# Optimization experiments

Hardware: AMD Instinct MI355X
Metric: run time of the kernel (lower is better)

Reference implementation:

```python
import jax, jax.numpy as jnp
import numpy as np

K = 5  # k_neighbors


def _pairwise_sq(a, b):
    # (B,N,3),(B,M,3) -> (B,N,M) squared euclidean distances (matmul form)
    d = (jnp.sum(a * a, -1)[:, :, None] + jnp.sum(b * b, -1)[:, None, :]
         - 2.0 * jnp.einsum('bnd,bmd->bnm', a, b))
    return jnp.maximum(d, 0.0)


def _knn_indices(points, k):
    # (B,N,3) -> (B,N,k) indices of k nearest neighbors, excluding self
    d = _pairwise_sq(points, points)
    _, idx = jax.lax.top_k(-d, k + 1)
    return idx[:, :, 1:]


def _gather_neighbors(feats, idx):
    # feats (B,N,C), idx (B,N,k) -> (B,N,k,C)
    B, N, k = idx.shape
    flat = jnp.take_along_axis(feats, idx.reshape(B, N * k, 1), axis=1)
    return flat.reshape(B, N, k, feats.shape[-1])


def setup_inputs() -> dict:
    key = jax.random.key(0)
    ks = jax.random.split(key, 8)
    B, N, M = 8, 4096, 4000
    return {
        'Y': jax.random.normal(ks[0], (B, N, 3), jnp.float32),
        'X': jax.random.normal(ks[1], (B, M, 3), jnp.float32),
        'R_pred': jax.random.normal(ks[2], (B, 3, 3), jnp.float32),
        't_pred': jax.random.normal(ks[3], (B, 3), jnp.float32),
        'R_gt': jax.random.normal(ks[4], (B, 3, 3), jnp.float32),
        't_gt': jax.random.normal(ks[5], (B, 3), jnp.float32),
        'X_hat': jax.random.normal(ks[6], (B, N, 3), jnp.float32),
        'delta': jax.random.normal(ks[7], (B, N, 3), jnp.float32),
    }


def reference(Y, X, R_pred, t_pred, R_gt, t_gt, X_hat, delta):
    lam_rot, lam_trans, lam_rmse = 1.0, 1.0, 1.0
    lam_align, lam_disp, lam_deform, lam_lap = 1.0, 0.01, 0.1, 0.1

    # --- rigid losses ---
    # rotation geodesic: R_delta = R_pred^T @ R_gt
    R_delta = jnp.einsum('bij,bik->bjk', R_pred, R_gt)
    tr = jnp.trace(R_delta, axis1=1, axis2=2)
    cos_a = jnp.clip((tr - 1.0) / 2.0, -1.0 + 1e-7, 1.0 - 1e-7)
    L_rot = jnp.mean(jnp.arccos(cos_a))

    L_trans = jnp.mean(jnp.linalg.norm(t_pred - t_gt, axis=1))

    # Y @ R^T + t
    Y_pred = jnp.einsum('bnd,bkd->bnk', Y, R_pred) + t_pred[:, None, :]
    Y_gt = jnp.einsum('bnd,bkd->bnk', Y, R_gt) + t_gt[:, None, :]
    L_rmse = jnp.mean(jnp.sqrt(jnp.mean(jnp.sum((Y_pred - Y_gt) ** 2, -1), axis=1)))

    rigid = lam_rot * L_rot + lam_trans * L_trans + lam_rmse * L_rmse

    # --- non-rigid losses ---
    Y_rigid = Y_pred  # apply_rigid_transform(Y, R_pred, t_pred)

    # alignment: N != M -> kNN matching of X_hat against X
    d_align = _pairwise_sq(X_hat, X)          # (B,N,M)
    knn_d = -jax.lax.top_k(-d_align, K)[0]    # (B,N,K) smallest distances
    L_align = jnp.mean(knn_d)

    L_disp = jnp.mean(jnp.sum(delta ** 2, -1))

    # kNN graph on Y_rigid (original builds it twice with identical result)
    idx = _knn_indices(Y_rigid, K)            # (B,N,K)

    Yn = _gather_neighbors(Y_rigid, idx)      # (B,N,K,3)
    Xn = _gather_neighbors(X_hat, idx)
    edge_diff = (Xn - X_hat[:, :, None, :]) - (Yn - Y_rigid[:, :, None, :])
    L_deform = jnp.mean(jnp.sum(edge_diff ** 2, -1))

    dn = _gather_neighbors(delta, idx)        # (B,N,K,3)
    lap = delta - jnp.mean(dn, axis=2)
    L_lap = jnp.mean(jnp.sum(lap ** 2, -1))

    non_rigid = (lam_align * L_align + lam_disp * L_disp
                 + lam_deform * L_deform + lam_lap * L_lap)
    total = rigid + non_rigid

    return jnp.stack([total, rigid, non_rigid, L_rot, L_trans, L_rmse,
                      L_align, L_disp, L_deform, L_lap])
```

## Files before the change

### kernel.cpp

```cpp
#include <hip/hip_runtime.h>
#include <math.h>

#define BB 8
#define NN 4096
#define MM 4000
#define KK 5
#define NWAVE 8
#define QG 128
#define CH 512
#define NPAD 4096
#define SCAN_BLOCKS ((NN / QG) * BB * 2)

#define ACC_ROT    0
#define ACC_TRANS  1
#define ACC_ALIGN  2
#define ACC_DISP   3
#define ACC_DEFORM 4
#define ACC_LAP    5
#define ACC_RMSE   6
#define ACC_COUNT  14

#define INFF __int_as_float(0x7F800000)

__device__ __forceinline__ float waveReduceSum(float v) {
#pragma unroll
    for (int off = 32; off > 0; off >>= 1) v += __shfl_down(v, off, 64);
    return v;
}

template<bool SELF, bool PACK>
__device__ __forceinline__ void proc1(float4 c, int midx, int q,
                                      float ca, float cbq, float cc,
                                      float& b0, float& b1, float& b2,
                                      float& b3, float& b4) {
    float sc = fmaf(c.x, ca, fmaf(c.y, cbq, fmaf(c.z, cc, c.w)));
    float v;
    if (PACK) {
        unsigned pk = (__float_as_uint(sc) & 0xFFFFF000u) | (unsigned)midx;
        v = __uint_as_float(pk);
        if (SELF) v = (midx == q) ? INFF : v;
    } else {
        v = sc;
    }
    float n0 = fminf(b0, v);
    float n1 = __builtin_amdgcn_fmed3f(v, b0, b1);
    float n2 = __builtin_amdgcn_fmed3f(v, b1, b2);
    float n3 = __builtin_amdgcn_fmed3f(v, b2, b3);
    float n4 = __builtin_amdgcn_fmed3f(v, b3, b4);
    b0 = n0; b1 = n1; b2 = n2; b3 = n3; b4 = n4;
}

template<bool SELF, bool PACK>
__device__ __forceinline__ void scanGlob2(const float4* __restrict__ cb, int tc,
                                          float a0, float b0c, float c0, int q0,
                                          float a1, float b1c, float c1, int q1,
                                          float& x0, float& x1, float& x2,
                                          float& x3, float& x4,
                                          float& y0, float& y1, float& y2,
                                          float& y3, float& y4) {
    float4 A[8], B[8];
#pragma unroll
    for (int j = 0; j < 8; ++j) A[j] = cb[tc + j];

    for (int t0 = 0; t0 < CH; t0 += 16) {
#pragma unroll
        for (int j = 0; j < 8; ++j) B[j] = cb[tc + t0 + 8 + j];
#pragma unroll
        for (int j = 0; j < 8; ++j) {
            proc1<SELF, PACK>(A[j], tc + t0 + j, q0, a0, b0c, c0, x0, x1, x2, x3, x4);
            proc1<SELF, PACK>(A[j], tc + t0 + j, q1, a1, b1c, c1, y0, y1, y2, y3, y4);
        }
        if (t0 + 16 < CH) {
#pragma unroll
            for (int j = 0; j < 8; ++j) A[j] = cb[tc + t0 + 16 + j];
        }
#pragma unroll
        for (int j = 0; j < 8; ++j) {
            proc1<SELF, PACK>(B[j], tc + t0 + 8 + j, q0, a0, b0c, c0, x0, x1, x2, x3, x4);
            proc1<SELF, PACK>(B[j], tc + t0 + 8 + j, q1, a1, b1c, c1, y0, y1, y2, y3, y4);
        }
    }
}

__global__ void k_prep(const float* __restrict__ Y, const float* __restrict__ X,
                       const float* __restrict__ Rp, const float* __restrict__ tp,
                       const float* __restrict__ Rg, const float* __restrict__ tg,
                       const float* __restrict__ dl,
                       float4* __restrict__ YrP, float4* __restrict__ XP,
                       float* __restrict__ acc) {
    int b = blockIdx.x >> 4;
    int n = ((blockIdx.x & 15) << 8) + threadIdx.x;
    size_t base = ((size_t)b * NN + n) * 3;
    float yx = Y[base + 0], yy = Y[base + 1], yz = Y[base + 2];

    float rp[9], rg[9], tpv[3], tgv[3];
#pragma unroll
    for (int i = 0; i < 9; ++i) { rp[i] = Rp[b * 9 + i]; rg[i] = Rg[b * 9 + i]; }
#pragma unroll
    for (int i = 0; i < 3; ++i) { tpv[i] = tp[b * 3 + i]; tgv[i] = tg[b * 3 + i]; }

    float p[3], dr2 = 0.f;
#pragma unroll
    for (int k = 0; k < 3; ++k) {
        float pv = fmaf(yx, rp[k * 3 + 0], fmaf(yy, rp[k * 3 + 1], fmaf(yz, rp[k * 3 + 2], tpv[k])));
        float gv = fmaf(yx, rg[k * 3 + 0], fmaf(yy, rg[k * 3 + 1], fmaf(yz, rg[k * 3 + 2], tgv[k])));
        p[k] = pv;
        float dd = pv - gv;
        dr2 = fmaf(dd, dd, dr2);
    }
    YrP[(size_t)b * NPAD + n] =
        make_float4(p[0], p[1], p[2], fmaf(p[0], p[0], fmaf(p[1], p[1], p[2] * p[2])));

    float4 xe;
    if (n < MM) {
        size_t xb = ((size_t)b * MM + n) * 3;
        float x0 = X[xb + 0], x1 = X[xb + 1], x2 = X[xb + 2];
        xe = make_float4(x0, x1, x2, fmaf(x0, x0, fmaf(x1, x1, x2 * x2)));
    } else {
        xe = make_float4(0.f, 0.f, 0.f, INFF);
    }
    XP[(size_t)b * NPAD + n] = xe;

    float d0 = dl[base + 0], d1 = dl[base + 1], d2 = dl[base + 2];
    float dsq = d0 * d0 + d1 * d1 + d2 * d2;

    dr2 = waveReduceSum(dr2);
    dsq = waveReduceSum(dsq);
    if ((threadIdx.x & 63) == 0) {
        atomicAdd(&acc[ACC_RMSE + b], dr2);
        atomicAdd(&acc[ACC_DISP], dsq);
    }

    if (threadIdx.x == 0 && (blockIdx.x & 15) == 0) {
        float tr = 0.f;
#pragma unroll
        for (int i = 0; i < 9; ++i) tr += rp[i] * rg[i];
        float c = (tr - 1.f) * 0.5f;
        c = fminf(fmaxf(c, -1.f + 1e-7f), 1.f - 1e-7f);
        float dx = tpv[0] - tgv[0], dy = tpv[1] - tgv[1], dz = tpv[2] - tgv[2];
        atomicAdd(&acc[ACC_ROT], acosf(c));
        atomicAdd(&acc[ACC_TRANS], sqrtf(dx * dx + dy * dy + dz * dz));
    }
}

__device__ void finalize(const float* acc, float* out) {
    float a[ACC_COUNT];
#pragma unroll
    for (int i = 0; i < ACC_COUNT; ++i)
        a[i] = __hip_atomic_load(&acc[i], __ATOMIC_RELAXED, __HIP_MEMORY_SCOPE_AGENT);
    float L_rot = a[ACC_ROT] / BB;
    float L_trans = a[ACC_TRANS] / BB;
    float L_rmse = 0.f;
#pragma unroll
    for (int b = 0; b < BB; ++b) L_rmse += sqrtf(a[ACC_RMSE + b] / NN);
    L_rmse /= BB;
    float L_align = a[ACC_ALIGN] / ((float)BB * NN * KK);
    float L_disp = a[ACC_DISP] / ((float)BB * NN);
    float L_def = a[ACC_DEFORM] / ((float)BB * NN * KK);
    float L_lap = a[ACC_LAP] / ((float)BB * NN);
    float rigid = L_rot + L_trans + L_rmse;
    float nr = L_align + 0.01f * L_disp + 0.1f * L_def + 0.1f * L_lap;
    out[0] = rigid + nr; out[1] = rigid; out[2] = nr;
    out[3] = L_rot; out[4] = L_trans; out[5] = L_rmse;
    out[6] = L_align; out[7] = L_disp; out[8] = L_def; out[9] = L_lap;
}

#define MERGE_STEP(W) { float d = md[W][l][pp##W]; if (d < best) { best = d; bw = W; } }
#define MERGE_ADV()  { pp0 += (bw == 0); pp1 += (bw == 1); pp2 += (bw == 2); pp3 += (bw == 3); \
                       pp4 += (bw == 4); pp5 += (bw == 5); pp6 += (bw == 6); pp7 += (bw == 7); }

__global__ __launch_bounds__(512, 4) void k_scan(const float* __restrict__ Xh,
                                                 const float4* __restrict__ XP,
                                                 const float4* __restrict__ YrP,
                                                 const float* __restrict__ dl,
                                                 float* __restrict__ acc,
                                                 unsigned* __restrict__ doneCnt,
                                                 float* __restrict__ out) {
    __shared__ float md[NWAVE][QG][6];
    int tid = threadIdx.x, wave = tid >> 6, lane = tid & 63;
    int qg = blockIdx.x, b = blockIdx.y, mode = blockIdx.z;
    int q0 = qg * QG + lane, q1 = q0 + 64;

    const float4* cbG = (mode == 0 ? XP : YrP) + (size_t)b * NPAD;

    float qx0, qy0, qz0, qx1, qy1, qz1;
    if (mode == 0) {
        size_t a0 = ((size_t)b * NN + q0) * 3;
        size_t a1 = ((size_t)b * NN + q1) * 3;
        qx0 = Xh[a0 + 0]; qy0 = Xh[a0 + 1]; qz0 = Xh[a0 + 2];
        qx1 = Xh[a1 + 0]; qy1 = Xh[a1 + 1]; qz1 = Xh[a1 + 2];
    } else {
        float4 p0 = cbG[q0], p1 = cbG[q1];
        qx0 = p0.x; qy0 = p0.y; qz0 = p0.z;
        qx1 = p1.x; qy1 = p1.y; qz1 = p1.z;
    }

    float x0 = INFF, x1 = INFF, x2 = INFF, x3 = INFF, x4 = INFF;
    float y0 = INFF, y1 = INFF, y2 = INFF, y3 = INFF, y4 = INFF;
    int tc = wave * CH;
    if (mode == 0) {
        scanGlob2<false, false>(cbG, tc,
                                -2.f * qx0, -2.f * qy0, -2.f * qz0, 0,
                                -2.f * qx1, -2.f * qy1, -2.f * qz1, 0,
                                x0, x1, x2, x3, x4, y0, y1, y2, y3, y4);
    } else if (wave == (qg >> 2)) {
        scanGlob2<true, true>(cbG, tc,
                              -2.f * qx0, -2.f * qy0, -2.f * qz0, q0,
                              -2.f * qx1, -2.f * qy1, -2.f * qz1, q1,
                              x0, x1, x2, x3, x4, y0, y1, y2, y3, y4);
    } else {
        scanGlob2<false, true>(cbG, tc,
                               -2.f * qx0, -2.f * qy0, -2.f * qz0, q0,
                               -2.f * qx1, -2.f * qy1, -2.f * qz1, q1,
                               x0, x1, x2, x3, x4, y0, y1, y2, y3, y4);
    }

    md[wave][lane][0] = x0; md[wave][lane][1] = x1; md[wave][lane][2] = x2;
    md[wave][lane][3] = x3; md[wave][lane][4] = x4; md[wave][lane][5] = INFF;
    md[wave][lane + 64][0] = y0; md[wave][lane + 64][1] = y1;
    md[wave][lane + 64][2] = y2; md[wave][lane + 64][3] = y3;
    md[wave][lane + 64][4] = y4; md[wave][lane + 64][5] = INFF;
    __syncthreads();

    if (tid < QG) {
        int l = tid;
        int q = qg * QG + l;
        int pp0 = 0, pp1 = 0, pp2 = 0, pp3 = 0, pp4 = 0, pp5 = 0, pp6 = 0, pp7 = 0;
        if (mode == 0) {
            size_t a0 = ((size_t)b * NN + q) * 3;
            float qx = Xh[a0 + 0], qy = Xh[a0 + 1], qz = Xh[a0 + 2];
            float qn = fmaf(qx, qx, fmaf(qy, qy, qz * qz));
            float s = 0.f;
#pragma unroll
            for (int k = 0; k < KK; ++k) {
                float best = INFF; int bw = 0;
                MERGE_STEP(0) MERGE_STEP(1) MERGE_STEP(2) MERGE_STEP(3)
                MERGE_STEP(4) MERGE_STEP(5) MERGE_STEP(6) MERGE_STEP(7)
                s += fmaxf(best + qn, 0.f);
                MERGE_ADV()
            }
            s = waveReduceSum(s);
            if ((l & 63) == 0) atomicAdd(&acc[ACC_ALIGN], s);
        } else {
            int si[KK];
#pragma unroll
            for (int k = 0; k < KK; ++k) {
                float best = INFF; int bw = 0;
                MERGE_STEP(0) MERGE_STEP(1) MERGE_STEP(2) MERGE_STEP(3)
                MERGE_STEP(4) MERGE_STEP(5) MERGE_STEP(6) MERGE_STEP(7)
                si[k] = (int)(__float_as_uint(best) & 0xFFFu);
                MERGE_ADV()
            }
            float4 qp = cbG[q];
            const float* xh = Xh + (size_t)b * NN * 3;
            const float* dlb = dl + (size_t)b * NN * 3;
            float xnx = xh[q * 3 + 0], xny = xh[q * 3 + 1], xnz = xh[q * 3 + 2];
            float dnx = dlb[q * 3 + 0], dny = dlb[q * 3 + 1], dnz = dlb[q * 3 + 2];

            float def = 0.f, sx = 0.f, sy = 0.f, sz = 0.f;
#pragma unroll
            for (int k = 0; k < KK; ++k) {
                int n = si[k];
                float4 yj = cbG[n];
                float ex = (xh[n * 3 + 0] - xnx) - (yj.x - qp.x);
                float ey = (xh[n * 3 + 1] - xny) - (yj.y - qp.y);
                float ez = (xh[n * 3 + 2] - xnz) - (yj.z - qp.z);
                def += ex * ex + ey * ey + ez * ez;
                sx += dlb[n * 3 + 0]; sy += dlb[n * 3 + 1]; sz += dlb[n * 3 + 2];
            }
            float lx = dnx - sx / 5.f, ly = dny - sy / 5.f, lz = dnz - sz / 5.f;
            float lap = lx * lx + ly * ly + lz * lz;

            def = waveReduceSum(def);
            lap = waveReduceSum(lap);
            if ((l & 63) == 0) {
                atomicAdd(&acc[ACC_DEFORM], def);
                atomicAdd(&acc[ACC_LAP], lap);
            }
        }
    }
    __syncthreads();
    if (tid == 0) {
        __threadfence();
        unsigned t = __hip_atomic_fetch_add(doneCnt, 1u, __ATOMIC_ACQ_REL,
                                            __HIP_MEMORY_SCOPE_AGENT);
        if (t == SCAN_BLOCKS - 1) finalize(acc, out);
    }
}

extern "C" void kernel_launch(void* const* d_in, const int* in_sizes, int n_in,
                              void* d_out, int out_size, void* d_ws, size_t ws_size,
                              hipStream_t stream) {
    const float* Y  = (const float*)d_in[0];
    const float* X  = (const float*)d_in[1];
    const float* Rp = (const float*)d_in[2];
    const float* tp = (const float*)d_in[3];
    const float* Rg = (const float*)d_in[4];
    const float* tg = (const float*)d_in[5];
    const float* Xh = (const float*)d_in[6];
    const float* dl = (const float*)d_in[7];
    float* out = (float*)d_out;

    float*    acc     = (float*)d_ws;
    unsigned* doneCnt = (unsigned*)((char*)d_ws + 64);
    float4*   YrP     = (float4*)((char*)d_ws + 512);
    float4*   XP      = YrP + (size_t)BB * NPAD;

    hipMemsetAsync(d_ws, 0, 512, stream);
    hipLaunchKernelGGL(k_prep, dim3(BB * NN / 256), dim3(256), 0, stream,
                       Y, X, Rp, tp, Rg, tg, dl, YrP, XP, acc);
    hipLaunchKernelGGL(k_scan, dim3(NN / QG, BB, 2), dim3(512), 0, stream,
                       Xh, XP, YrP, dl, acc, doneCnt, out);
}
```

Before: 118.5 us.

## Stage candidate points in LDS in two halves and merge partial top-5 lists

The candidate-point scan now reads from shared memory instead of global memory. Each block cooperatively loads half of the candidate set (2048 float4) into LDS, all eight waves scan their 256-point slices, and the per-wave top-5 lists are merged and folded into a running top-5 with a branchless two-list merge. The intent is to cut redundant global/L2 traffic, since every wave in every block previously re-read the whole candidate array. In exchange the kernel adds 32KB of LDS per block, which may limit occupancy, plus extra barriers and two merge passes.

```diff
diff --git a/kernel.cpp b/kernel.cpp
--- a/kernel.cpp
+++ b/kernel.cpp
@@ -7,7 +7,8 @@
 #define KK 5
 #define NWAVE 8
 #define QG 128
-#define CH 512
+#define CH 256
+#define HSZ 2048
 #define NPAD 4096
 #define SCAN_BLOCKS ((NN / QG) * BB * 2)
 
@@ -51,35 +52,50 @@
 }
 
 template<bool SELF, bool PACK>
-__device__ __forceinline__ void scanGlob2(const float4* __restrict__ cb, int tc,
-                                          float a0, float b0c, float c0, int q0,
-                                          float a1, float b1c, float c1, int q1,
-                                          float& x0, float& x1, float& x2,
-                                          float& x3, float& x4,
-                                          float& y0, float& y1, float& y2,
-                                          float& y3, float& y4) {
-    float4 A[8], B[8];
-#pragma unroll
-    for (int j = 0; j < 8; ++j) A[j] = cb[tc + j];
-
-    for (int t0 = 0; t0 < CH; t0 += 16) {
-#pragma unroll
-        for (int j = 0; j < 8; ++j) B[j] = cb[tc + t0 + 8 + j];
-#pragma unroll
-        for (int j = 0; j < 8; ++j) {
-            proc1<SELF, PACK>(A[j], tc + t0 + j, q0, a0, b0c, c0, x0, x1, x2, x3, x4);
-            proc1<SELF, PACK>(A[j], tc + t0 + j, q1, a1, b1c, c1, y0, y1, y2, y3, y4);
-        }
-        if (t0 + 16 < CH) {
-#pragma unroll
-            for (int j = 0; j < 8; ++j) A[j] = cb[tc + t0 + 16 + j];
-        }
-#pragma unroll
-        for (int j = 0; j < 8; ++j) {
-            proc1<SELF, PACK>(B[j], tc + t0 + 8 + j, q0, a0, b0c, c0, x0, x1, x2, x3, x4);
-            proc1<SELF, PACK>(B[j], tc + t0 + 8 + j, q1, a1, b1c, c1, y0, y1, y2, y3, y4);
-        }
-    }
+__device__ __forceinline__ void scanLDS2(const float4* lc, int tl, int tg,
+                                         float a0, float b0c, float c0, int q0,
+                                         float a1, float b1c, float c1, int q1,
+                                         float& x0, float& x1, float& x2,
+                                         float& x3, float& x4,
+                                         float& y0, float& y1, float& y2,
+                                         float& y3, float& y4) {
+    float4 A[4], B[4];
+#pragma unroll
+    for (int j = 0; j < 4; ++j) A[j] = lc[tl + j];
+
+    for (int t0 = 0; t0 < CH; t0 += 8) {
+#pragma unroll
+        for (int j = 0; j < 4; ++j) B[j] = lc[tl + t0 + 4 + j];
+#pragma unroll
+        for (int j = 0; j < 4; ++j) {
+            proc1<SELF, PACK>(A[j], tg + t0 + j, q0, a0, b0c, c0, x0, x1, x2, x3, x4);
+            proc1<SELF, PACK>(A[j], tg + t0 + j, q1, a1, b1c, c1, y0, y1, y2, y3, y4);
+        }
+        if (t0 + 8 < CH) {
+#pragma unroll
+            for (int j = 0; j < 4; ++j) A[j] = lc[tl + t0 + 8 + j];
+        }
+#pragma unroll
+        for (int j = 0; j < 4; ++j) {
+            proc1<SELF, PACK>(B[j], tg + t0 + 4 + j, q0, a0, b0c, c0, x0, x1, x2, x3, x4);
+            proc1<SELF, PACK>(B[j], tg + t0 + 4 + j, q1, a1, b1c, c1, y0, y1, y2, y3, y4);
+        }
+    }
+}
+
+__device__ __forceinline__ void merge5(float& a0, float& a1, float& a2,
+                                       float& a3, float& a4,
+                                       float m0, float m1, float m2,
+                                       float m3, float m4) {
+    float u0 = fminf(a0, m0);
+    float u1 = fminf(fminf(a1, m1), fmaxf(a0, m0));
+    float u2 = fminf(fminf(a2, m2), fminf(fmaxf(a0, m1), fmaxf(a1, m0)));
+    float u3 = fminf(fminf(a3, m3),
+                     fminf(fmaxf(a0, m2), fminf(fmaxf(a1, m1), fmaxf(a2, m0))));
+    float u4 = fminf(fminf(a4, m4),
+                     fminf(fminf(fmaxf(a0, m3), fmaxf(a1, m2)),
+                           fminf(fmaxf(a2, m1), fmaxf(a3, m0))));
+    a0 = u0; a1 = u1; a2 = u2; a3 = u3; a4 = u4;
 }
 
 __global__ void k_prep(const float* __restrict__ Y, const float* __restrict__ X,
@@ -176,6 +192,7 @@
                                                  float* __restrict__ acc,
                                                  unsigned* __restrict__ doneCnt,
                                                  float* __restrict__ out) {
+    __shared__ float4 stage[HSZ];
     __shared__ float md[NWAVE][QG][6];
     int tid = threadIdx.x, wave = tid >> 6, lane = tid & 63;
     int qg = blockIdx.x, b = blockIdx.y, mode = blockIdx.z;
@@ -195,62 +212,80 @@
         qx1 = p1.x; qy1 = p1.y; qz1 = p1.z;
     }
 
-    float x0 = INFF, x1 = INFF, x2 = INFF, x3 = INFF, x4 = INFF;
-    float y0 = INFF, y1 = INFF, y2 = INFF, y3 = INFF, y4 = INFF;
-    int tc = wave * CH;
-    if (mode == 0) {
-        scanGlob2<false, false>(cbG, tc,
-                                -2.f * qx0, -2.f * qy0, -2.f * qz0, 0,
-                                -2.f * qx1, -2.f * qy1, -2.f * qz1, 0,
-                                x0, x1, x2, x3, x4, y0, y1, y2, y3, y4);
-    } else if (wave == (qg >> 2)) {
-        scanGlob2<true, true>(cbG, tc,
-                              -2.f * qx0, -2.f * qy0, -2.f * qz0, q0,
-                              -2.f * qx1, -2.f * qy1, -2.f * qz1, q1,
-                              x0, x1, x2, x3, x4, y0, y1, y2, y3, y4);
-    } else {
-        scanGlob2<false, true>(cbG, tc,
-                               -2.f * qx0, -2.f * qy0, -2.f * qz0, q0,
-                               -2.f * qx1, -2.f * qy1, -2.f * qz1, q1,
-                               x0, x1, x2, x3, x4, y0, y1, y2, y3, y4);
-    }
-
-    md[wave][lane][0] = x0; md[wave][lane][1] = x1; md[wave][lane][2] = x2;
-    md[wave][lane][3] = x3; md[wave][lane][4] = x4; md[wave][lane][5] = INFF;
-    md[wave][lane + 64][0] = y0; md[wave][lane + 64][1] = y1;
-    md[wave][lane + 64][2] = y2; md[wave][lane + 64][3] = y3;
-    md[wave][lane + 64][4] = y4; md[wave][lane + 64][5] = INFF;
-    __syncthreads();
+    float f0 = INFF, f1 = INFF, f2 = INFF, f3 = INFF, f4 = INFF;
+
+#pragma unroll
+    for (int half = 0; half < 2; ++half) {
+        __syncthreads();
+#pragma unroll
+        for (int i = 0; i < HSZ / 512; ++i)
+            stage[tid + i * 512] = cbG[half * HSZ + tid + i * 512];
+        __syncthreads();
+
+        float x0 = INFF, x1 = INFF, x2 = INFF, x3 = INFF, x4 = INFF;
+        float y0 = INFF, y1 = INFF, y2 = INFF, y3 = INFF, y4 = INFF;
+        int tl = wave * CH;
+        int tg = half * HSZ + tl;
+        bool hasSelf = (mode == 1) && (half == (qg >> 4)) && (wave == ((qg >> 1) & 7));
+        if (mode == 0) {
+            scanLDS2<false, false>(stage, tl, tg,
+                                   -2.f * qx0, -2.f * qy0, -2.f * qz0, 0,
+                                   -2.f * qx1, -2.f * qy1, -2.f * qz1, 0,
+                                   x0, x1, x2, x3, x4, y0, y1, y2, y3, y4);
+        } else if (hasSelf) {
+            scanLDS2<true, true>(stage, tl, tg,
+                                 -2.f * qx0, -2.f * qy0, -2.f * qz0, q0,
+                                 -2.f * qx1, -2.f * qy1, -2.f * qz1, q1,
+                                 x0, x1, x2, x3, x4, y0, y1, y2, y3, y4);
+        } else {
+            scanLDS2<false, true>(stage, tl, tg,
+                                  -2.f * qx0, -2.f * qy0, -2.f * qz0, q0,
+                                  -2.f * qx1, -2.f * qy1, -2.f * qz1, q1,
+                                  x0, x1, x2, x3, x4, y0, y1, y2, y3, y4);
+        }
+
+        md[wave][lane][0] = x0; md[wave][lane][1] = x1; md[wave][lane][2] = x2;
+        md[wave][lane][3] = x3; md[wave][lane][4] = x4; md[wave][lane][5] = INFF;
+        md[wave][lane + 64][0] = y0; md[wave][lane + 64][1] = y1;
+        md[wave][lane + 64][2] = y2; md[wave][lane + 64][3] = y3;
+        md[wave][lane + 64][4] = y4; md[wave][lane + 64][5] = INFF;
+        __syncthreads();
+
+        if (tid < QG) {
+            int l = tid;
+            int pp0 = 0, pp1 = 0, pp2 = 0, pp3 = 0, pp4 = 0, pp5 = 0, pp6 = 0, pp7 = 0;
+            float m5[KK];
+#pragma unroll
+            for (int k = 0; k < KK; ++k) {
+                float best = INFF; int bw = 0;
+                MERGE_STEP(0) MERGE_STEP(1) MERGE_STEP(2) MERGE_STEP(3)
+                MERGE_STEP(4) MERGE_STEP(5) MERGE_STEP(6) MERGE_STEP(7)
+                m5[k] = best;
+                MERGE_ADV()
+            }
+            merge5(f0, f1, f2, f3, f4, m5[0], m5[1], m5[2], m5[3], m5[4]);
+        }
+    }
 
     if (tid < QG) {
         int l = tid;
         int q = qg * QG + l;
-        int pp0 = 0, pp1 = 0, pp2 = 0, pp3 = 0, pp4 = 0, pp5 = 0, pp6 = 0, pp7 = 0;
         if (mode == 0) {
             size_t a0 = ((size_t)b * NN + q) * 3;
             float qx = Xh[a0 + 0], qy = Xh[a0 + 1], qz = Xh[a0 + 2];
             float qn = fmaf(qx, qx, fmaf(qy, qy, qz * qz));
-            float s = 0.f;
-#pragma unroll
-            for (int k = 0; k < KK; ++k) {
-                float best = INFF; int bw = 0;
-                MERGE_STEP(0) MERGE_STEP(1) MERGE_STEP(2) MERGE_STEP(3)
-                MERGE_STEP(4) MERGE_STEP(5) MERGE_STEP(6) MERGE_STEP(7)
-                s += fmaxf(best + qn, 0.f);
-                MERGE_ADV()
-            }
+            float s = fmaxf(f0 + qn, 0.f) + fmaxf(f1 + qn, 0.f) + fmaxf(f2 + qn, 0.f)
+                    + fmaxf(f3 + qn, 0.f) + fmaxf(f4 + qn, 0.f);
             s = waveReduceSum(s);
             if ((l & 63) == 0) atomicAdd(&acc[ACC_ALIGN], s);
         } else {
             int si[KK];
-#pragma unroll
-            for (int k = 0; k < KK; ++k) {
-                float best = INFF; int bw = 0;
-                MERGE_STEP(0) MERGE_STEP(1) MERGE_STEP(2) MERGE_STEP(3)
-                MERGE_STEP(4) MERGE_STEP(5) MERGE_STEP(6) MERGE_STEP(7)
-                si[k] = (int)(__float_as_uint(best) & 0xFFFu);
-                MERGE_ADV()
-            }
+            si[0] = (int)(__float_as_uint(f0) & 0xFFFu);
+            si[1] = (int)(__float_as_uint(f1) & 0xFFFu);
+            si[2] = (int)(__float_as_uint(f2) & 0xFFFu);
+            si[3] = (int)(__float_as_uint(f3) & 0xFFFu);
+            si[4] = (int)(__float_as_uint(f4) & 0xFFFu);
+
             float4 qp = cbG[q];
             const float* xh = Xh + (size_t)b * NN * 3;
             const float* dlb = dl + (size_t)b * NN * 3;
```

Result: faster. 108.4 us (median of 2 runs) (-8.5%).
